# Optimization experiments

Measured on AMD Instinct MI355X. Metric: run time of the kernel, lower is better.

Reference implementation:

```python
import jax, jax.numpy as jnp
import numpy as np

B, S, H = 2, 1024, 4096
NH, NKV, D = 32, 8, 128
EPS = 1e-6
THETA = 10000.0


def rotate_half(x):
    x1, x2 = jnp.split(x, 2, axis=-1)
    return jnp.concatenate([-x2, x1], axis=-1)


def rmsnorm(x, w, eps):
    # RMSNorm over the last (head_dim) axis
    var = jnp.mean(x * x, axis=-1, keepdims=True)
    return x * jax.lax.rsqrt(var + eps) * w


def setup_inputs() -> dict:
    key = jax.random.key(0)
    ks = jax.random.split(key, 6)
    hidden_states = jax.random.normal(ks[0], (B, S, H), dtype=jnp.float32)
    # scaled init so activations stay O(1)
    Wq = jax.random.normal(ks[1], (NH * D, H), dtype=jnp.float32) * (H ** -0.5)
    Wk = jax.random.normal(ks[2], (NKV * D, H), dtype=jnp.float32) * (H ** -0.5)
    Wv = jax.random.normal(ks[3], (NKV * D, H), dtype=jnp.float32) * (H ** -0.5)
    Wo = jax.random.normal(ks[4], (H, NH * D), dtype=jnp.float32) * ((NH * D) ** -0.5)
    q_norm_w = jnp.ones((D,), dtype=jnp.float32)
    k_norm_w = jnp.ones((D,), dtype=jnp.float32)
    # standard default RoPE cos/sin tables, broadcast to [B, S, D]
    pos = jnp.arange(S, dtype=jnp.float32)
    inv_freq = 1.0 / (THETA ** (jnp.arange(0, D, 2, dtype=jnp.float32) / D))
    freqs = pos[:, None] * inv_freq[None, :]            # [S, D/2]
    emb = jnp.concatenate([freqs, freqs], axis=-1)      # [S, D]
    cos = jnp.broadcast_to(jnp.cos(emb)[None], (B, S, D)).astype(jnp.float32)
    sin = jnp.broadcast_to(jnp.sin(emb)[None], (B, S, D)).astype(jnp.float32)
    return dict(hidden_states=hidden_states, cos=cos, sin=sin,
                Wq=Wq, Wk=Wk, Wv=Wv, Wo=Wo,
                q_norm_w=q_norm_w, k_norm_w=k_norm_w)


def reference(hidden_states, cos, sin, Wq, Wk, Wv, Wo, q_norm_w, k_norm_w):
    b, s, h = hidden_states.shape
    # fused QKV projections (MojoLinear: y = x @ W.T, no bias)
    q = (hidden_states @ Wq.T).reshape(b, s, NH, D)
    k = (hidden_states @ Wk.T).reshape(b, s, NKV, D)
    v = (hidden_states @ Wv.T).reshape(b, s, NKV, D)
    # per-head-dim RMSNorm on q and k, then [B, H, S, D] layout
    q = rmsnorm(q, q_norm_w, EPS).transpose(0, 2, 1, 3)   # [B, NH,  S, D]
    k = rmsnorm(k, k_norm_w, EPS).transpose(0, 2, 1, 3)   # [B, NKV, S, D]
    v = v.transpose(0, 2, 1, 3)                           # [B, NKV, S, D]
    # RoPE (rotate-half)
    c = cos[:, None, :, :]
    sn = sin[:, None, :, :]
    q = q * c + rotate_half(q) * sn
    k = k * c + rotate_half(k) * sn
    # GQA: expand KV heads to query heads
    groups = NH // NKV
    k = jnp.repeat(k, groups, axis=1)                     # [B, NH, S, D]
    v = jnp.repeat(v, groups, axis=1)
    # causal attention (prefill with empty paged cache == causal SDPA)
    scores = jnp.einsum('bhqd,bhkd->bhqk', q, k) * (D ** -0.5)
    causal = jnp.tril(jnp.ones((s, s), dtype=bool))
    scores = jnp.where(causal, scores, jnp.finfo(scores.dtype).min)
    probs = jax.nn.softmax(scores, axis=-1)
    out = jnp.einsum('bhqk,bhkd->bhqd', probs, v)         # [B, NH, S, D]
    out = out.transpose(0, 2, 1, 3).reshape(b, s, NH * D)
    return out @ Wo.T
```

## Files before the change

### kernel.cpp

```cpp
#include <hip/hip_runtime.h>


typedef float  f32x4   __attribute__((ext_vector_type(4)));
typedef float  f32x16  __attribute__((ext_vector_type(16)));
typedef __bf16 bf16x8  __attribute__((ext_vector_type(8)));
typedef unsigned short u16x8 __attribute__((ext_vector_type(8)));

__device__ __forceinline__ unsigned short f2b(float f) {
    union { float f; unsigned int u; } x;
    x.f = f;
    unsigned int u = x.u;
    unsigned int r = u + 0x7fffu + ((u >> 16) & 1u);
    return (unsigned short)(r >> 16);
}

__device__ __forceinline__ void async16(const unsigned short* g, unsigned short* l) {
    __builtin_amdgcn_global_load_lds(
        (const __attribute__((address_space(1))) void*)g,
        (__attribute__((address_space(3))) void*)l, 16, 0, 0);
}

__global__ __launch_bounds__(256) void cvt(const float* __restrict__ s,
                                           unsigned short* __restrict__ d, int n8) {
    int i = blockIdx.x * 256 + threadIdx.x;
    if (i >= n8) return;
    const float4* s4 = (const float4*)s + (size_t)i * 2;
    float4 a = s4[0], b = s4[1];
    u16x8 o;
    o[0] = f2b(a.x); o[1] = f2b(a.y); o[2] = f2b(a.z); o[3] = f2b(a.w);
    o[4] = f2b(b.x); o[5] = f2b(b.y); o[6] = f2b(b.z); o[7] = f2b(b.w);
    *((u16x8*)d + i) = o;
}

__global__ __launch_bounds__(256) void gemm_bt_bf16(const unsigned short* __restrict__ A,
                                                    const unsigned short* __restrict__ W,
                                                    float* __restrict__ C,
                                                    int K, int N) {
    __shared__ __align__(16) unsigned short As[128 * 64];
    __shared__ __align__(16) unsigned short Bs[128 * 64];

    const int tid  = threadIdx.x;
    const int wave = tid >> 6, lane = tid & 63;
    const int wm   = wave >> 1, wn = wave & 1;
    const int l31  = lane & 31, lh = lane >> 5;
    const int arow = blockIdx.y * 128, brow = blockIdx.x * 128;

    int rr[4], gc[4], slot[4];
    #pragma unroll
    for (int it = 0; it < 4; it++) {
        slot[it] = it * 4 + wave;
        int ci = slot[it] * 64 + lane;
        rr[it] = ci >> 3;
        int c  = ci & 7;
        gc[it] = c ^ (rr[it] & 7);
    }

    f32x16 acc[2][2] = {};

    for (int k0 = 0; k0 < K; k0 += 64) {
        #pragma unroll
        for (int it = 0; it < 4; it++) {
            async16(A + (size_t)(arow + rr[it]) * K + k0 + gc[it] * 8, &As[slot[it] * 512]);
            async16(W + (size_t)(brow + rr[it]) * K + k0 + gc[it] * 8, &Bs[slot[it] * 512]);
        }
        __syncthreads();

        bf16x8 af[4][2], bfr[4][2];
        #pragma unroll
        for (int ks = 0; ks < 4; ks++) {
            #pragma unroll
            for (int i = 0; i < 2; i++) {
                int rowa = wm * 64 + i * 32 + l31;
                int ch   = (ks * 2 + lh) ^ (rowa & 7);
                af[ks][i]  = *(const bf16x8*)&As[rowa * 64 + ch * 8];
                int rowb = wn * 64 + i * 32 + l31;
                int chb  = (ks * 2 + lh) ^ (rowb & 7);
                bfr[ks][i] = *(const bf16x8*)&Bs[rowb * 64 + chb * 8];
            }
        }
        #pragma unroll
        for (int ks = 0; ks < 4; ks++)
            #pragma unroll
            for (int i = 0; i < 2; i++)
                #pragma unroll
                for (int j = 0; j < 2; j++)
                    acc[i][j] = __builtin_amdgcn_mfma_f32_32x32x16_bf16(af[ks][i], bfr[ks][j], acc[i][j], 0, 0, 0);
        __syncthreads();
    }

    #pragma unroll
    for (int i = 0; i < 2; i++)
        #pragma unroll
        for (int j = 0; j < 2; j++)
            #pragma unroll
            for (int r = 0; r < 16; r++) {
                int row = arow + wm * 64 + i * 32 + lh * 4 + (r & 3) + 8 * (r >> 2);
                int col = brow + wn * 64 + j * 32 + l31;
                C[(size_t)row * N + col] = acc[i][j][r];
            }
}

__global__ __launch_bounds__(256) void norm_rope(const float* __restrict__ X, int rstride,
                                                 const float* __restrict__ cosp,
                                                 const float* __restrict__ sinp,
                                                 const float* __restrict__ w,
                                                 unsigned short* __restrict__ Y, int nh) {
    const int wid  = blockIdx.x * 4 + (threadIdx.x >> 6);
    const int lane = threadIdx.x & 63;
    const int row  = wid / nh;
    const int h    = wid - row * nh;

    const float* xp = X + (size_t)row * rstride + h * 128;
    float x0 = xp[lane], x1 = xp[lane + 64];
    float ss = x0 * x0 + x1 * x1;
    #pragma unroll
    for (int off = 32; off; off >>= 1) ss += __shfl_xor(ss, off, 64);
    float r = rsqrtf(ss * (1.0f / 128.0f) + 1e-6f);
    float n0 = x0 * r * w[lane];
    float n1 = x1 * r * w[lane + 64];
    const float* cp = cosp + (size_t)row * 128;
    const float* sp = sinp + (size_t)row * 128;
    float y0 = n0 * cp[lane]      - n1 * sp[lane];
    float y1 = n1 * cp[lane + 64] + n0 * sp[lane + 64];
    const int b = row >> 10, s = row & 1023;
    unsigned short* yp = Y + (((size_t)(b * nh + h)) * 1024 + s) * 128;
    yp[lane]      = f2b(y0);
    yp[lane + 64] = f2b(y1);
}

__global__ __launch_bounds__(256) void v_trans(const float* __restrict__ V,
                                               unsigned short* __restrict__ Vt) {
    __shared__ float T[64][65];
    const int tid = threadIdx.x;
    const int st = blockIdx.x >> 1, dt = blockIdx.x & 1;
    const int bh = blockIdx.y, b = bh >> 3, h = bh & 7;

    const int sl = tid >> 2, c0 = (tid & 3) * 16;
    const float* src = V + (size_t)(b * 1024 + st * 64 + sl) * 6144 + h * 128 + dt * 64 + c0;
    #pragma unroll
    for (int j = 0; j < 4; j++) {
        float4 v = *(const float4*)(src + j * 4);
        *(float4*)&T[sl][c0 + j * 4] = v;
    }
    __syncthreads();

    const int dgrp = tid >> 6, sl2 = tid & 63;
    unsigned short* dst = Vt + (size_t)bh * 131072 + st * 64 + sl2;
    #pragma unroll
    for (int jd = 0; jd < 16; jd++) {
        int dl = dgrp * 16 + jd;
        dst[(size_t)(dt * 64 + dl) * 1024] = f2b(T[sl2][dl]);
    }
}

__global__ __launch_bounds__(256) void attn(const unsigned short* __restrict__ Qb,
                                            const unsigned short* __restrict__ Kb,
                                            const unsigned short* __restrict__ Vt,
                                            unsigned short* __restrict__ Ob) {
    __shared__ __align__(16) unsigned short Klds[128 * 128];
    __shared__ __align__(16) unsigned short Plds[4][16][136];

    const int tid  = threadIdx.x;
    const int w    = tid >> 6, lane = tid & 63;
    const int quad = lane >> 4, l15 = lane & 15;
    const int h = blockIdx.y, b = blockIdx.z, kvh = h >> 2;

    const unsigned short* Qp = Qb + ((size_t)(b * 32 + h))   * 131072;
    const unsigned short* Kp = Kb + ((size_t)(b * 8 + kvh))  * 131072;
    const unsigned short* Vp = Vt + ((size_t)(b * 8 + kvh))  * 131072;
    const float c2 = (float)(0.08838834764831845 * 1.4426950408889634);

    for (int half = 0; half < 2; half++) {
        const int qt = half ? (15 - (int)blockIdx.x) : (int)blockIdx.x;
        const int q0 = qt * 64;
        const int qrow = q0 + w * 16 + l15;

        bf16x8 qf[4];
        #pragma unroll
        for (int ks = 0; ks < 4; ks++)
            qf[ks] = *(const bf16x8*)(Qp + (size_t)qrow * 128 + ks * 32 + quad * 8);

        float m_i[4], l_i[4];
        #pragma unroll
        for (int r = 0; r < 4; r++) { m_i[r] = -1e30f; l_i[r] = 0.0f; }
        f32x4 o[8] = {};

        const int ntiles = (qt >> 1) + 1;
        const int nfull  = (qt * 64 + 1) >> 7;

        for (int kt = 0; kt < ntiles; kt++) {
            __syncthreads();
            #pragma unroll
            for (int it = 0; it < 8; it++) {
                int slot = it * 4 + w;
                int ci = slot * 64 + lane;
                int r = ci >> 4, c = ci & 15;
                int g = (c & 8) | ((c ^ r) & 7);
                async16(Kp + (size_t)(kt * 128 + r) * 128 + g * 8, &Klds[slot * 512]);
            }
            __syncthreads();

            f32x4 sacc[8] = {};
            #pragma unroll
            for (int ks = 0; ks < 4; ks++) {
                #pragma unroll
                for (int tn = 0; tn < 8; tn++) {
                    int row = tn * 16 + l15;
                    int ch  = ks * 4 + quad;
                    int chs = (ch & 8) | ((ch ^ row) & 7);
                    bf16x8 kf = *(const bf16x8*)&Klds[row * 128 + chs * 8];
                    sacc[tn] = __builtin_amdgcn_mfma_f32_16x16x32_bf16(qf[ks], kf, sacc[tn], 0, 0, 0);
                }
            }

            const bool masked = (kt >= nfull);
            #pragma unroll
            for (int r = 0; r < 4; r++) {
                float sv[8];
                float rmax = -1e30f;
                if (masked) {
                    const int qg = q0 + w * 16 + quad * 4 + r;
                    #pragma unroll
                    for (int tn = 0; tn < 8; tn++) {
                        float v = sacc[tn][r];
                        int kg = kt * 128 + tn * 16 + l15;
                        if (kg > qg) v = -1e30f;
                        sv[tn] = v;
                        rmax = fmaxf(rmax, v);
                    }
                } else {
                    #pragma unroll
                    for (int tn = 0; tn < 8; tn++) {
                        sv[tn] = sacc[tn][r];
                        rmax = fmaxf(rmax, sv[tn]);
                    }
                }
                #pragma unroll
                for (int off = 8; off; off >>= 1) rmax = fmaxf(rmax, __shfl_xor(rmax, off, 16));
                float mnew  = fmaxf(m_i[r], rmax);
                float alpha = __builtin_amdgcn_exp2f((m_i[r] - mnew) * c2);
                float rsum  = 0.0f;
                #pragma unroll
                for (int tn = 0; tn < 8; tn++) {
                    float p = __builtin_amdgcn_exp2f((sv[tn] - mnew) * c2);
                    sv[tn] = p;
                    rsum += p;
                }
                #pragma unroll
                for (int off = 8; off; off >>= 1) rsum += __shfl_xor(rsum, off, 16);
                m_i[r] = mnew;
                l_i[r] = l_i[r] * alpha + rsum;
                #pragma unroll
                for (int td = 0; td < 8; td++) o[td][r] *= alpha;
                #pragma unroll
                for (int tn = 0; tn < 8; tn++)
                    Plds[w][quad * 4 + r][tn * 16 + l15] = f2b(sv[tn]);
            }

            #pragma unroll
            for (int ks = 0; ks < 4; ks++) {
                bf16x8 pf = *(const bf16x8*)&Plds[w][l15][ks * 32 + quad * 8];
                #pragma unroll
                for (int td = 0; td < 8; td++) {
                    bf16x8 vf = *(const bf16x8*)(Vp + (size_t)(td * 16 + l15) * 1024 + kt * 128 + ks * 32 + quad * 8);
                    o[td] = __builtin_amdgcn_mfma_f32_16x16x32_bf16(pf, vf, o[td], 0, 0, 0);
                }
            }
        }

        #pragma unroll
        for (int r = 0; r < 4; r++) {
            float inv = 1.0f / l_i[r];
            const int qg = q0 + w * 16 + quad * 4 + r;
            unsigned short* op = Ob + ((size_t)(b * 1024 + qg)) * 4096 + h * 128;
            #pragma unroll
            for (int td = 0; td < 8; td++)
                op[td * 16 + l15] = f2b(o[td][r] * inv);
        }
    }
}

extern "C" void kernel_launch(void* const* d_in, const int* in_sizes, int n_in,
                              void* d_out, int out_size, void* d_ws, size_t ws_size,
                              hipStream_t stream) {
    const float* hid  = (const float*)d_in[0];
    const float* cosp = (const float*)d_in[1];
    const float* sinp = (const float*)d_in[2];
    const float* Wq   = (const float*)d_in[3];
    const float* Wk   = (const float*)d_in[4];
    const float* Wv   = (const float*)d_in[5];
    const float* Wo   = (const float*)d_in[6];
    const float* qw   = (const float*)d_in[7];
    const float* kw   = (const float*)d_in[8];
    float* out = (float*)d_out;

    char* ws = (char*)d_ws;
    float* QKVf = (float*)ws;
    unsigned short* Ob = (unsigned short*)ws;
    size_t off = (size_t)2048 * 6144 * 4;
    unsigned short* hidb  = (unsigned short*)(ws + off); off += (size_t)2048 * 4096 * 2;
    unsigned short* Wqkvb = (unsigned short*)(ws + off); off += (size_t)6144 * 4096 * 2;
    unsigned short* Wob   = (unsigned short*)(ws + off); off += (size_t)4096 * 4096 * 2;
    unsigned short* Qb    = (unsigned short*)(ws + off); off += (size_t)2048 * 4096 * 2;
    unsigned short* Kb    = (unsigned short*)(ws + off); off += (size_t)2048 * 1024 * 2;
    unsigned short* Vt    = (unsigned short*)(ws + off);

    dim3 blk(256);
    cvt<<<4096, blk, 0, stream>>>(hid, hidb, 1048576);
    cvt<<<8192, blk, 0, stream>>>(Wq, Wqkvb, 2097152);
    cvt<<<2048, blk, 0, stream>>>(Wk, Wqkvb + (size_t)4096 * 4096, 524288);
    cvt<<<2048, blk, 0, stream>>>(Wv, Wqkvb + (size_t)5120 * 4096, 524288);
    cvt<<<8192, blk, 0, stream>>>(Wo, Wob, 2097152);
    gemm_bt_bf16<<<dim3(48, 16), blk, 0, stream>>>(hidb, Wqkvb, QKVf, 4096, 6144);
    norm_rope<<<16384, blk, 0, stream>>>(QKVf,        6144, cosp, sinp, qw, Qb, 32);
    norm_rope<<<4096,  blk, 0, stream>>>(QKVf + 4096, 6144, cosp, sinp, kw, Kb, 8);
    v_trans<<<dim3(32, 16), blk, 0, stream>>>(QKVf + 5120, Vt);
    attn<<<dim3(8, 32, 2), blk, 0, stream>>>(Qb, Kb, Vt, Ob);
    gemm_bt_bf16<<<dim3(32, 16), blk, 0, stream>>>(Ob, Wob, out, 4096, 4096);
}
```

Measured before the change: 512.1 us.

## Add 256x192 pipelined QKV GEMM, merge conversions, raise MFMA priority

```diff
diff --git a/kernel.cpp b/kernel.cpp
--- a/kernel.cpp
+++ b/kernel.cpp
@@ -20,16 +20,136 @@
         (__attribute__((address_space(3))) void*)l, 16, 0, 0);
 }
 
-__global__ __launch_bounds__(256) void cvt(const float* __restrict__ s,
-                                           unsigned short* __restrict__ d, int n8) {
+__global__ __launch_bounds__(256) void cvt_all(const float* __restrict__ hsrc,
+                                               const float* __restrict__ wq,
+                                               const float* __restrict__ wk,
+                                               const float* __restrict__ wv,
+                                               const float* __restrict__ wo,
+                                               unsigned short* __restrict__ hidb,
+                                               unsigned short* __restrict__ wqkvb,
+                                               unsigned short* __restrict__ wob) {
     int i = blockIdx.x * 256 + threadIdx.x;
-    if (i >= n8) return;
-    const float4* s4 = (const float4*)s + (size_t)i * 2;
+    if (i >= 6291456) return;
+    const float* s; unsigned short* d; int j;
+    if (i < 1048576)      { s = hsrc; d = hidb;             j = i; }
+    else if (i < 3145728) { s = wq;   d = wqkvb;            j = i - 1048576; }
+    else if (i < 3670016) { s = wk;   d = wqkvb + 16777216; j = i - 3145728; }
+    else if (i < 4194304) { s = wv;   d = wqkvb + 20971520; j = i - 3670016; }
+    else                  { s = wo;   d = wob;              j = i - 4194304; }
+    const float4* s4 = (const float4*)s + (size_t)j * 2;
     float4 a = s4[0], b = s4[1];
     u16x8 o;
     o[0] = f2b(a.x); o[1] = f2b(a.y); o[2] = f2b(a.z); o[3] = f2b(a.w);
     o[4] = f2b(b.x); o[5] = f2b(b.y); o[6] = f2b(b.z); o[7] = f2b(b.w);
-    *((u16x8*)d + i) = o;
+    *((u16x8*)d + j) = o;
+}
+
+__global__ __launch_bounds__(512, 2) void gemm256_bt(const unsigned short* __restrict__ A,
+                                                     const unsigned short* __restrict__ W,
+                                                     float* __restrict__ C,
+                                                     int K, int N) {
+    __shared__ __align__(16) unsigned short Ab[3][256 * 64];
+    __shared__ __align__(16) unsigned short Bb[2][192 * 64];
+
+    const int tid  = threadIdx.x;
+    const int wave = tid >> 6, lane = tid & 63;
+    const int wm   = wave >> 2, wn = wave & 3;
+    const int l15  = lane & 15, h = lane >> 4;
+    const int cx0  = (h ^ (l15 & 7)) << 3;
+    const int cx1  = cx0 ^ 32;
+    const int stgrow = wave * 8 + (lane >> 3);
+    const int stgcol = ((lane & 7) ^ (lane >> 3)) << 3;
+    const int aRow0 = blockIdx.y * 256;
+    const int bRow0 = blockIdx.x * 192;
+    const int NT = K >> 6;
+
+#define STAGE_A(t, s, bi) async16(A + (size_t)(aRow0 + (s)*64 + stgrow) * K + (t)*64 + stgcol, \
+                                  &Ab[bi][(s)*4096 + wave*512])
+#define STAGE_B(t, s, bi) async16(W + (size_t)(bRow0 + (s)*64 + stgrow) * K + (t)*64 + stgcol, \
+                                  &Bb[bi][(s)*4096 + wave*512])
+#define LOAD_AQ(q) do { \
+    _Pragma("unroll") \
+    for (int mi = 0; mi < 2; mi++) { \
+        const unsigned short* ap = Ab_ + (wm * 128 + (q) * 32 + mi * 16 + l15) * 64; \
+        af[mi][0] = *(const bf16x8*)(ap + cx0); \
+        af[mi][1] = *(const bf16x8*)(ap + cx1); \
+    } } while (0)
+#define MFMA_Q(q) do { \
+    _Pragma("unroll") \
+    for (int mi = 0; mi < 2; mi++) \
+    _Pragma("unroll") \
+    for (int nf = 0; nf < 3; nf++) { \
+        acc[(q)*2+mi][nf] = __builtin_amdgcn_mfma_f32_16x16x32_bf16(af[mi][0], bfr[nf][0], acc[(q)*2+mi][nf], 0, 0, 0); \
+        acc[(q)*2+mi][nf] = __builtin_amdgcn_mfma_f32_16x16x32_bf16(af[mi][1], bfr[nf][1], acc[(q)*2+mi][nf], 0, 0, 0); \
+    } } while (0)
+#define BARRIER() __builtin_amdgcn_s_barrier()
+#define LGKM0()   asm volatile("s_waitcnt lgkmcnt(0)" ::: "memory")
+
+    f32x4 acc[8][3] = {};
+
+    STAGE_B(0, 0, 0); STAGE_B(0, 1, 0); STAGE_B(0, 2, 0);
+    STAGE_A(0, 0, 0); STAGE_A(0, 1, 0); STAGE_A(0, 2, 0); STAGE_A(0, 3, 0);
+    STAGE_A(1, 0, 1); STAGE_A(1, 1, 1); STAGE_A(1, 2, 1); STAGE_A(1, 3, 1);
+    asm volatile("s_waitcnt vmcnt(4)" ::: "memory");
+    BARRIER();
+
+    for (int t = 0; t < NT; ++t) {
+        const unsigned short* Ab_ = Ab[t % 3];
+        const unsigned short* Bb_ = Bb[t & 1];
+        const int rb1 = (t & 1) ^ 1, ra2 = (t + 2) % 3;
+        const bool sb = (t + 1 < NT), sa = (t + 2 < NT);
+        bf16x8 af[2][2], bfr[3][2];
+
+        #pragma unroll
+        for (int nf = 0; nf < 3; nf++) {
+            const unsigned short* bp = Bb_ + (wn * 48 + nf * 16 + l15) * 64;
+            bfr[nf][0] = *(const bf16x8*)(bp + cx0);
+            bfr[nf][1] = *(const bf16x8*)(bp + cx1);
+        }
+        LOAD_AQ(0);
+        if (sb) { STAGE_B(t + 1, 0, rb1); STAGE_B(t + 1, 1, rb1); }
+        BARRIER(); LGKM0();
+        __builtin_amdgcn_s_setprio(1); MFMA_Q(0); __builtin_amdgcn_s_setprio(0);
+        BARRIER();
+
+        LOAD_AQ(1);
+        if (sb) STAGE_B(t + 1, 2, rb1);
+        if (sa) STAGE_A(t + 2, 0, ra2);
+        BARRIER(); LGKM0();
+        __builtin_amdgcn_s_setprio(1); MFMA_Q(1); __builtin_amdgcn_s_setprio(0);
+        BARRIER();
+
+        LOAD_AQ(2);
+        if (sa) { STAGE_A(t + 2, 1, ra2); STAGE_A(t + 2, 2, ra2); }
+        BARRIER(); LGKM0();
+        __builtin_amdgcn_s_setprio(1); MFMA_Q(2); __builtin_amdgcn_s_setprio(0);
+        BARRIER();
+
+        LOAD_AQ(3);
+        if (sa) STAGE_A(t + 2, 3, ra2);
+        if (sa) asm volatile("s_waitcnt vmcnt(4)" ::: "memory");
+        else    asm volatile("s_waitcnt vmcnt(0)" ::: "memory");
+        BARRIER(); LGKM0();
+        __builtin_amdgcn_s_setprio(1); MFMA_Q(3); __builtin_amdgcn_s_setprio(0);
+        BARRIER();
+    }
+
+    #pragma unroll
+    for (int mf = 0; mf < 8; mf++)
+        #pragma unroll
+        for (int nf = 0; nf < 3; nf++)
+            #pragma unroll
+            for (int r = 0; r < 4; r++) {
+                int row = aRow0 + wm * 128 + mf * 16 + h * 4 + r;
+                int col = bRow0 + wn * 48 + nf * 16 + l15;
+                C[(size_t)row * N + col] = acc[mf][nf][r];
+            }
+#undef STAGE_A
+#undef STAGE_B
+#undef LOAD_AQ
+#undef MFMA_Q
+#undef BARRIER
+#undef LGKM0
 }
 
 __global__ __launch_bounds__(256) void gemm_bt_bf16(const unsigned short* __restrict__ A,
@@ -201,6 +321,7 @@
             __syncthreads();
 
             f32x4 sacc[8] = {};
+            __builtin_amdgcn_s_setprio(1);
             #pragma unroll
             for (int ks = 0; ks < 4; ks++) {
                 #pragma unroll
@@ -212,6 +333,7 @@
                     sacc[tn] = __builtin_amdgcn_mfma_f32_16x16x32_bf16(qf[ks], kf, sacc[tn], 0, 0, 0);
                 }
             }
+            __builtin_amdgcn_s_setprio(0);
 
             const bool masked = (kt >= nfull);
             #pragma unroll
@@ -257,6 +379,7 @@
                     Plds[w][quad * 4 + r][tn * 16 + l15] = f2b(sv[tn]);
             }
 
+            __builtin_amdgcn_s_setprio(1);
             #pragma unroll
             for (int ks = 0; ks < 4; ks++) {
                 bf16x8 pf = *(const bf16x8*)&Plds[w][l15][ks * 32 + quad * 8];
@@ -266,6 +389,7 @@
                     o[td] = __builtin_amdgcn_mfma_f32_16x16x32_bf16(pf, vf, o[td], 0, 0, 0);
                 }
             }
+            __builtin_amdgcn_s_setprio(0);
         }
 
         #pragma unroll
@@ -306,12 +430,8 @@
     unsigned short* Vt    = (unsigned short*)(ws + off);
 
     dim3 blk(256);
-    cvt<<<4096, blk, 0, stream>>>(hid, hidb, 1048576);
-    cvt<<<8192, blk, 0, stream>>>(Wq, Wqkvb, 2097152);
-    cvt<<<2048, blk, 0, stream>>>(Wk, Wqkvb + (size_t)4096 * 4096, 524288);
-    cvt<<<2048, blk, 0, stream>>>(Wv, Wqkvb + (size_t)5120 * 4096, 524288);
-    cvt<<<8192, blk, 0, stream>>>(Wo, Wob, 2097152);
-    gemm_bt_bf16<<<dim3(48, 16), blk, 0, stream>>>(hidb, Wqkvb, QKVf, 4096, 6144);
+    cvt_all<<<24576, blk, 0, stream>>>(hid, Wq, Wk, Wv, Wo, hidb, Wqkvb, Wob);
+    gemm256_bt<<<dim3(32, 8), dim3(512), 0, stream>>>(hidb, Wqkvb, QKVf, 4096, 6144);
     norm_rope<<<16384, blk, 0, stream>>>(QKVf,        6144, cosp, sinp, qw, Qb, 32);
     norm_rope<<<4096,  blk, 0, stream>>>(QKVf + 4096, 6144, cosp, sinp, kw, Kb, 8);
     v_trans<<<dim3(32, 16), blk, 0, stream>>>(QKVf + 5120, Vt);
```

Result: no change. 518.2 us (+1.2%).
